# Kernel tuning notes

Measured on AMD Instinct MI355X. Metric: run time of the kernel, lower is better.

Reference implementation:

```python
import jax, jax.numpy as jnp
import numpy as np

R = 0.25
M = 0


def setup_inputs() -> dict:
    key = jax.random.key(0)
    k1, k2, k3, k4 = jax.random.split(key, 4)
    B, T_cmp, C = 2, 4096, 4096
    H, KVH, D, W = 32, 8, 128, 512
    return {
        "x_m": jax.random.normal(k1, (B, 2 * T_cmp, C), dtype=jnp.float32),
        "xm_cmp": jax.random.normal(k2, (B, T_cmp, C), dtype=jnp.float32),
        "q_w": jax.random.normal(k3, (B, H, W, D), dtype=jnp.float32),
        "km_cmp": jax.random.normal(k4, (B, KVH, T_cmp, D), dtype=jnp.float32),
    }


def reference(x_m, xm_cmp, q_w, km_cmp):
    B, T_cmp, C = xm_cmp.shape
    groups = q_w.shape[1] // km_cmp.shape[1]  # GQA repeat factor
    scaling = q_w.shape[-1] ** -0.5

    # importance_score: repeat kv heads, scaled-dot attention, softmax over keys,
    # sum over query positions, mean over heads -> [B, T_cmp]
    km = jnp.repeat(km_cmp, groups, axis=1)  # [B, H, T_cmp, D]
    scores = jnp.einsum('bhqd,bhkd->bhqk', q_w, km) * scaling
    weights = jax.nn.softmax(scores, axis=-1)
    importance = weights.sum(axis=2).mean(axis=1)  # [B, T_cmp]

    # select_indices: static top-k count
    k = min(int(R * T_cmp + M * (1 - R) / 2), T_cmp)
    _, idx = jax.lax.top_k(importance, k)  # [B, k]

    # interleave_selected: selected compressed tokens are replaced by their
    # two original tokens x_m[2t], x_m[2t+1]; others keep xm_cmp[t].
    b_idx = jnp.arange(B)[:, None]
    expand_mask = jnp.zeros((B, T_cmp), dtype=bool).at[b_idx, idx].set(True)
    sizes = jnp.where(expand_mask, 2, 1)
    start = jnp.cumsum(sizes, axis=1) - sizes  # output start position per token
    T_out = T_cmp + k

    first = jnp.where(expand_mask[..., None], x_m[:, ::2], xm_cmp)  # [B,T_cmp,C]
    second = x_m[:, 1::2]  # [B, T_cmp, C]
    pos2 = jnp.where(expand_mask, start + 1, T_out)  # non-expanded -> dummy slot

    y = jnp.zeros((B, T_out + 1, C), dtype=xm_cmp.dtype)
    y = y.at[b_idx, start].set(first)
    y = y.at[b_idx, pos2].set(second)
    return y[:, :T_out]
```

## Files before the change

kernel.cpp:

```cpp
#include <hip/hip_runtime.h>
#include <hip/hip_bf16.h>

#define B_    2
#define H_    32
#define KVH_  8
#define T_    4096
#define C_    4096
#define D_    128
#define W_    512
#define KTOP  1024
#define TOUT  (T_ + KTOP)
#define QB    64
#define NQB   (W_/QB)
#define TB    64
#define NTT   (T_/TB)
#define NPART (H_*NQB)
#define NBLK  (NQB*H_*B_)
#define SCALE 0.08838834764831845f

typedef __attribute__((ext_vector_type(8))) _Float16 half8;
typedef __attribute__((ext_vector_type(4))) float f32x4;

__device__ __forceinline__ void gload16(const void* g, void* l) {
    __builtin_amdgcn_global_load_lds(
        (const __attribute__((address_space(1))) void*)g,
        (__attribute__((address_space(3))) void*)l, 16, 0, 0);
}

__global__ __launch_bounds__(256) void convert_k_kernel(
    const float* __restrict__ km, _Float16* __restrict__ Khw,
    _Float16* __restrict__ Klw)
{
    int g = blockIdx.x*256 + threadIdx.x;
    size_t e = (size_t)g*8;
    int d0 = (int)(e & 127);
    size_t row = e >> 7;
    int t = (int)(row & (T_-1));
    size_t bk = row >> 12;
    int r = t & 63, tt = t >> 6;
    size_t off = (bk<<19) + (size_t)tt*(TB*D_) + (size_t)r*D_ + (d0 ^ ((r&7)<<3));
    float4 v0 = *(const float4*)(km + e);
    float4 v1 = *(const float4*)(km + e + 4);
    float f[8] = {v0.x,v0.y,v0.z,v0.w,v1.x,v1.y,v1.z,v1.w};
    half8 hh, hl;
#pragma unroll
    for (int i = 0; i < 8; ++i) {
        _Float16 hi = (_Float16)f[i];
        hh[i] = hi;
        hl[i] = (_Float16)(f[i] - (float)hi);
    }
    *(half8*)&Khw[off] = hh;
    *(half8*)&Klw[off] = hl;
}

#define STAGE_W(bufidx, tt)                                                 \
    {                                                                       \
        const _Float16* gh_ = gh0 + (size_t)(tt)*8192;                      \
        const _Float16* gl_ = gl0 + (size_t)(tt)*8192;                      \
        gload16(gh_,        &sKh[bufidx][wid][lane*8]);                     \
        gload16(gh_ + 512,  &sKh[bufidx][wid][512 + lane*8]);               \
        gload16(gh_ + 1024, &sKh[bufidx][wid][1024 + lane*8]);              \
        gload16(gh_ + 1536, &sKh[bufidx][wid][1536 + lane*8]);              \
        gload16(gl_,        &sKl[bufidx][wid][lane*8]);                     \
        gload16(gl_ + 512,  &sKl[bufidx][wid][512 + lane*8]);               \
        gload16(gl_ + 1024, &sKl[bufidx][wid][1024 + lane*8]);              \
        gload16(gl_ + 1536, &sKl[bufidx][wid][1536 + lane*8]);              \
    }

#define TILE_MFMA(bufidx, acc)                                              \
    {                                                                       \
        const _Float16* bKh = sKh[bufidx][wid];                             \
        const _Float16* bKl = sKl[bufidx][wid];                             \
        __builtin_amdgcn_s_setprio(1);                                      \
        _Pragma("unroll")                                                   \
        for (int ks2 = 0; ks2 < 4; ++ks2) {                                 \
            const int off = li*D_ + ((ks2*32 + lg*8) ^ ((li & 7) << 3));    \
            half8 bh = *(const half8*)&bKh[off];                            \
            half8 bl = *(const half8*)&bKl[off];                            \
            _Pragma("unroll")                                               \
            for (int mm = 0; mm < 4; ++mm) {                                \
                acc[mm] = __builtin_amdgcn_mfma_f32_16x16x32_f16(qh[mm][ks2], bh, acc[mm], 0,0,0); \
                acc[mm] = __builtin_amdgcn_mfma_f32_16x16x32_f16(ql[mm][ks2], bh, acc[mm], 0,0,0); \
                acc[mm] = __builtin_amdgcn_mfma_f32_16x16x32_f16(qh[mm][ks2], bl, acc[mm], 0,0,0); \
            }                                                               \
        }                                                                   \
        __builtin_amdgcn_s_setprio(0);                                      \
    }

__global__ __launch_bounds__(256, 2) void fused_imp_kernel(
    const float* __restrict__ q_w, const _Float16* __restrict__ Khw,
    const _Float16* __restrict__ Klw, float* __restrict__ partial)
{
    __shared__ __align__(16) _Float16 sKh[2][4][16*D_];
    __shared__ __align__(16) _Float16 sKl[2][4][16*D_];
    __shared__ float sL[4][QB];
    __shared__ float sR[QB];

    const int tid = threadIdx.x, wid = tid >> 6, lane = tid & 63;
    const int lg = lane >> 4, li = lane & 15;
    const int kg = wid;

    const int flat = blockIdx.x;
    const int xcd = flat & 7, m = flat >> 3;
    const int g = (m >> 5)*8 + xcd;
    const int r = m & 31;
    const int kvh = g & 7, b = g >> 3;
    const int hh = r >> 3, qb = r & 7;
    const int h = kvh*4 + hh;

    half8 qh[4][4], ql[4][4];
    {
        const float* qp0 = q_w + (((size_t)b*H_ + h)*W_ + qb*QB + li)*D_;
#pragma unroll
        for (int mm = 0; mm < 4; ++mm)
#pragma unroll
            for (int ks2 = 0; ks2 < 4; ++ks2) {
                const float* p = qp0 + mm*16*D_ + ks2*32 + lg*8;
                float4 v0 = *(const float4*)p;
                float4 v1 = *(const float4*)(p+4);
                float f[8] = {v0.x,v0.y,v0.z,v0.w,v1.x,v1.y,v1.z,v1.w};
#pragma unroll
                for (int e = 0; e < 8; ++e) {
                    _Float16 hv = (_Float16)f[e];
                    qh[mm][ks2][e] = hv;
                    ql[mm][ks2][e] = (_Float16)(f[e] - (float)hv);
                }
            }
    }

    const size_t kvoff = ((size_t)b*KVH_ + kvh) * ((size_t)T_*D_);
    const _Float16* gh0 = Khw + kvoff + (size_t)wid*2048 + (size_t)lane*8;
    const _Float16* gl0 = Klw + kvoff + (size_t)wid*2048 + (size_t)lane*8;

    float lacc[4][4] = {};
    STAGE_W(0, 0);
    int cur = 0;
    for (int tt = 0; tt < NTT; ++tt) {
        if (tt + 1 < NTT) {
            STAGE_W(cur^1, tt+1);
            asm volatile("s_waitcnt vmcnt(8)" ::: "memory");
        } else {
            asm volatile("s_waitcnt vmcnt(0)" ::: "memory");
        }
        f32x4 acc[4];
#pragma unroll
        for (int mm = 0; mm < 4; ++mm) acc[mm] = (f32x4){0.f,0.f,0.f,0.f};
        TILE_MFMA(cur, acc);
#pragma unroll
        for (int mm = 0; mm < 4; ++mm)
#pragma unroll
            for (int j = 0; j < 4; ++j)
                lacc[mm][j] += __expf(acc[mm][j]*SCALE);
        cur ^= 1;
    }
#pragma unroll
    for (int mm = 0; mm < 4; ++mm)
#pragma unroll
        for (int j = 0; j < 4; ++j) {
            float v = lacc[mm][j];
            v += __shfl_xor(v, 1); v += __shfl_xor(v, 2);
            v += __shfl_xor(v, 4); v += __shfl_xor(v, 8);
            if (li == 0) sL[kg][mm*16 + lg*4 + j] = v;
        }
    __syncthreads();
    if (tid < QB) {
        float l = sL[0][tid] + sL[1][tid] + sL[2][tid] + sL[3][tid];
        sR[tid] = 1.0f / l;
    }
    __syncthreads();
    float rv[4][4];
#pragma unroll
    for (int mm = 0; mm < 4; ++mm)
#pragma unroll
        for (int j = 0; j < 4; ++j)
            rv[mm][j] = sR[mm*16 + lg*4 + j];

    const size_t po = (((size_t)(h*NQB + qb))*B_ + b)*T_;
    STAGE_W(0, 0);
    cur = 0;
    for (int tt = 0; tt < NTT; ++tt) {
        if (tt == 0) {
            STAGE_W(cur^1, 1);
            asm volatile("s_waitcnt vmcnt(8)" ::: "memory");
        } else if (tt + 1 < NTT) {
            STAGE_W(cur^1, tt+1);
            asm volatile("s_waitcnt vmcnt(9)" ::: "memory");
        } else {
            asm volatile("s_waitcnt vmcnt(1)" ::: "memory");
        }
        f32x4 acc[4];
#pragma unroll
        for (int mm = 0; mm < 4; ++mm) acc[mm] = (f32x4){0.f,0.f,0.f,0.f};
        TILE_MFMA(cur, acc);
        float x = 0.f;
#pragma unroll
        for (int mm = 0; mm < 4; ++mm)
#pragma unroll
            for (int j = 0; j < 4; ++j)
                x += __expf(acc[mm][j]*SCALE)*rv[mm][j];
        x += __shfl_xor(x, 16); x += __shfl_xor(x, 32);
        if (lg == 0)
            partial[po + (size_t)tt*TB + kg*16 + li] = x;
        cur ^= 1;
    }
}

__global__ __launch_bounds__(256) void imp_reduce_kernel(
    const float* __restrict__ partial, float* __restrict__ imp)
{
    int gid = blockIdx.x*256 + threadIdx.x;
    int b = gid >> 12, t = gid & (T_-1);
    float s = 0.f;
    for (int i = 0; i < NPART; ++i)
        s += partial[((size_t)(i*B_ + b))*T_ + t];
    imp[gid] = s * (1.0f/H_);
}

__global__ __launch_bounds__(1024) void topk_kernel(
    const float* __restrict__ imp, int* __restrict__ mask, int* __restrict__ start)
{
    __shared__ int hist[256];
    __shared__ int sa[1024], sb[1024];
    __shared__ int sbin, srem;
    const int tid = threadIdx.x, b = blockIdx.x;
    const int i0 = 4*tid;

    unsigned key[4];
#pragma unroll
    for (int j = 0; j < 4; ++j) {
        unsigned u = __float_as_uint(imp[b*T_ + i0 + j]);
        key[j] = (u & 0x80000000u) ? ~u : (u | 0x80000000u);
    }

    unsigned prefix = 0;
    int k_rem = KTOP;
#pragma unroll
    for (int sh = 24; sh >= 0; sh -= 8) {
        unsigned hi_mask = (sh == 24) ? 0u : (0xFFFFFFFFu << (sh + 8));
        if (tid < 256) hist[tid] = 0;
        __syncthreads();
#pragma unroll
        for (int j = 0; j < 4; ++j)
            if ((key[j] & hi_mask) == prefix)
                atomicAdd(&hist[(key[j] >> sh) & 255], 1);
        __syncthreads();
        if (tid == 0) {
            int acc = 0, bin = 255;
            for (; bin > 0; --bin) {
                int hv = hist[bin];
                if (acc + hv >= k_rem) break;
                acc += hv;
            }
            sbin = bin; srem = k_rem - acc;
        }
        __syncthreads();
        prefix |= ((unsigned)sbin) << sh;
        k_rem = srem;
        __syncthreads();
    }

    int m[4], eq[4];
#pragma unroll
    for (int j = 0; j < 4; ++j) {
        m[j]  = key[j] > prefix ? 1 : 0;
        eq[j] = (key[j] == prefix) ? 1 : 0;
    }
    int e4 = eq[0]+eq[1]+eq[2]+eq[3];
    sa[tid] = e4;
    __syncthreads();
    {
        int *src = sa, *dst = sb;
        for (int off = 1; off < 1024; off <<= 1) {
            int v = src[tid];
            if (tid >= off) v += src[tid - off];
            dst[tid] = v;
            __syncthreads();
            int* t2 = src; src = dst; dst = t2;
        }
        int r = src[tid] - e4;
#pragma unroll
        for (int j = 0; j < 4; ++j) {
            if (eq[j] && r < k_rem) m[j] = 1;
            r += eq[j];
        }
    }
    __syncthreads();
    int s4 = m[0]+m[1]+m[2]+m[3];
    sa[tid] = s4;
    __syncthreads();
    int *src = sa, *dst = sb;
    for (int off = 1; off < 1024; off <<= 1) {
        int v = src[tid];
        if (tid >= off) v += src[tid - off];
        dst[tid] = v;
        __syncthreads();
        int* t2 = src; src = dst; dst = t2;
    }
    int excl = src[tid] - s4;
    start[b*T_+i0+0] = i0+0 + excl;
    start[b*T_+i0+1] = i0+1 + excl + m[0];
    start[b*T_+i0+2] = i0+2 + excl + m[0]+m[1];
    start[b*T_+i0+3] = i0+3 + excl + m[0]+m[1]+m[2];
    mask[b*T_+i0+0] = m[0]; mask[b*T_+i0+1] = m[1];
    mask[b*T_+i0+2] = m[2]; mask[b*T_+i0+3] = m[3];
}

__global__ __launch_bounds__(256) void scatter_kernel(
    const float* __restrict__ x_m, const float* __restrict__ xm_cmp,
    const int* __restrict__ mask, const int* __restrict__ start,
    float* __restrict__ out)
{
    const int t = blockIdx.x, b = blockIdx.y, tid = threadIdx.x;
    const int mk = mask[b*T_+t];
    const int st = start[b*T_+t];
    const float* s1 = mk ? (x_m + ((size_t)b*2*T_ + 2*t)*C_)
                         : (xm_cmp + ((size_t)b*T_ + t)*C_);
    float4* d1 = (float4*)(out + ((size_t)b*TOUT + st)*C_);
    const float4* s1v = (const float4*)s1;
    for (int i = tid; i < C_/4; i += 256) d1[i] = s1v[i];
    if (mk) {
        const float4* s2v = (const float4*)(x_m + ((size_t)b*2*T_ + 2*t+1)*C_);
        float4* d2 = d1 + C_/4;
        for (int i = tid; i < C_/4; i += 256) d2[i] = s2v[i];
    }
}

extern "C" void kernel_launch(void* const* d_in, const int* in_sizes, int n_in,
                              void* d_out, int out_size, void* d_ws, size_t ws_size,
                              hipStream_t stream)
{
    (void)in_sizes; (void)n_in; (void)out_size; (void)ws_size;
    const float* x_m    = (const float*)d_in[0];
    const float* xm_cmp = (const float*)d_in[1];
    const float* q_w    = (const float*)d_in[2];
    const float* km     = (const float*)d_in[3];
    float* out = (float*)d_out;

    char* ws = (char*)d_ws;
    _Float16* Khw   = (_Float16*)ws;
    _Float16* Klw   = (_Float16*)(ws + 16777216);
    float* partial  = (float*)(ws + 33554432);
    float* imp      = (float*)(ws + 41943040);
    int*   mask     = (int*)  (ws + 41975808);
    int*   start    = (int*)  (ws + 42008576);

    convert_k_kernel<<<dim3(4096), dim3(256), 0, stream>>>(km, Khw, Klw);
    fused_imp_kernel<<<dim3(NBLK), dim3(256), 0, stream>>>(q_w, Khw, Klw, partial);
    imp_reduce_kernel<<<dim3((B_*T_)/256), dim3(256), 0, stream>>>(partial, imp);
    topk_kernel<<<dim3(B_), dim3(1024), 0, stream>>>(imp, mask, start);
    scatter_kernel<<<dim3(T_, B_), dim3(256), 0, stream>>>(x_m, xm_cmp, mask, start, out);
}
```

Before: 314.0 us.

## Pipeline exp against MFMA, fold scale into Q, drop low-K term in pass one

Both passes of the fused importance kernel are software-pipelined with two accumulator sets, so the exponentials for tile t-1 overlap the MFMAs of tile t. The softmax scale times log2(e) is folded into the fp16 split of Q at load time, which lets the inner loops call raw exp2 with no per-element multiply. The normalizer pass now uses only the high half of K: it loads half the K data and issues two MFMAs per step instead of three. This reduces load traffic and MFMA work in that pass. The risk is a small precision mismatch between the denominator and the three-term second pass.

```diff
diff --git a/kernel.cpp b/kernel.cpp
--- a/kernel.cpp
+++ b/kernel.cpp
@@ -16,7 +16,7 @@
 #define NTT   (T_/TB)
 #define NPART (H_*NQB)
 #define NBLK  (NQB*H_*B_)
-#define SCALE 0.08838834764831845f
+#define SLOG2E 0.12751744f
 
 typedef __attribute__((ext_vector_type(8))) _Float16 half8;
 typedef __attribute__((ext_vector_type(4))) float f32x4;
@@ -53,7 +53,16 @@
     *(half8*)&Klw[off] = hl;
 }
 
-#define STAGE_W(bufidx, tt)                                                 \
+#define STAGE1(bufidx, tt)                                                  \
+    {                                                                       \
+        const _Float16* gh_ = gh0 + (size_t)(tt)*8192;                      \
+        gload16(gh_,        &sKh[bufidx][wid][lane*8]);                     \
+        gload16(gh_ + 512,  &sKh[bufidx][wid][512 + lane*8]);               \
+        gload16(gh_ + 1024, &sKh[bufidx][wid][1024 + lane*8]);              \
+        gload16(gh_ + 1536, &sKh[bufidx][wid][1536 + lane*8]);              \
+    }
+
+#define STAGE2(bufidx, tt)                                                  \
     {                                                                       \
         const _Float16* gh_ = gh0 + (size_t)(tt)*8192;                      \
         const _Float16* gl_ = gl0 + (size_t)(tt)*8192;                      \
@@ -67,7 +76,25 @@
         gload16(gl_ + 1536, &sKl[bufidx][wid][1536 + lane*8]);              \
     }
 
-#define TILE_MFMA(bufidx, acc)                                              \
+#define MFMA2(bufidx, acc)                                                  \
+    {                                                                       \
+        const _Float16* bKh = sKh[bufidx][wid];                             \
+        __builtin_amdgcn_s_setprio(1);                                      \
+        _Pragma("unroll")                                                   \
+        for (int ks2 = 0; ks2 < 4; ++ks2) {                                 \
+            const int off = li*D_ + ((ks2*32 + lg*8) ^ ((li & 7) << 3));    \
+            half8 bh = *(const half8*)&bKh[off];                            \
+            _Pragma("unroll")                                               \
+            for (int mm = 0; mm < 4; ++mm)                                  \
+                acc[mm] = __builtin_amdgcn_mfma_f32_16x16x32_f16(qh[mm][ks2], bh, acc[mm], 0,0,0); \
+            _Pragma("unroll")                                               \
+            for (int mm = 0; mm < 4; ++mm)                                  \
+                acc[mm] = __builtin_amdgcn_mfma_f32_16x16x32_f16(ql[mm][ks2], bh, acc[mm], 0,0,0); \
+        }                                                                   \
+        __builtin_amdgcn_s_setprio(0);                                      \
+    }
+
+#define MFMA3(bufidx, acc)                                                  \
     {                                                                       \
         const _Float16* bKh = sKh[bufidx][wid];                             \
         const _Float16* bKl = sKl[bufidx][wid];                             \
@@ -78,14 +105,57 @@
             half8 bh = *(const half8*)&bKh[off];                            \
             half8 bl = *(const half8*)&bKl[off];                            \
             _Pragma("unroll")                                               \
-            for (int mm = 0; mm < 4; ++mm) {                                \
+            for (int mm = 0; mm < 4; ++mm)                                  \
                 acc[mm] = __builtin_amdgcn_mfma_f32_16x16x32_f16(qh[mm][ks2], bh, acc[mm], 0,0,0); \
+            _Pragma("unroll")                                               \
+            for (int mm = 0; mm < 4; ++mm)                                  \
                 acc[mm] = __builtin_amdgcn_mfma_f32_16x16x32_f16(ql[mm][ks2], bh, acc[mm], 0,0,0); \
+            _Pragma("unroll")                                               \
+            for (int mm = 0; mm < 4; ++mm)                                  \
                 acc[mm] = __builtin_amdgcn_mfma_f32_16x16x32_f16(qh[mm][ks2], bl, acc[mm], 0,0,0); \
-            }                                                               \
         }                                                                   \
         __builtin_amdgcn_s_setprio(0);                                      \
     }
+
+#define EXPACC(acc)                                                         \
+    _Pragma("unroll")                                                       \
+    for (int mm = 0; mm < 4; ++mm)                                          \
+        _Pragma("unroll")                                                   \
+        for (int j = 0; j < 4; ++j)                                         \
+            lacc[mm][j] += __builtin_amdgcn_exp2f(acc[mm][j]);
+
+#define EXPSTORE(acc, t)                                                    \
+    {                                                                       \
+        float x = 0.f;                                                      \
+        _Pragma("unroll")                                                   \
+        for (int mm = 0; mm < 4; ++mm)                                      \
+            _Pragma("unroll")                                               \
+            for (int j = 0; j < 4; ++j)                                     \
+                x += __builtin_amdgcn_exp2f(acc[mm][j]) * rv[mm][j];        \
+        x += __shfl_xor(x, 16); x += __shfl_xor(x, 32);                     \
+        if (lg == 0)                                                        \
+            partial[po + (size_t)(t)*TB + kg*16 + li] = x;                  \
+    }
+
+#define P1BODY(t, ACCD, ACCE)                                               \
+    {                                                                       \
+        STAGE1(((t)+1) & 1, (t)+1);                                         \
+        asm volatile("s_waitcnt vmcnt(4)" ::: "memory");                    \
+        MFMA2((t) & 1, ACCD);                                               \
+        EXPACC(ACCE);                                                       \
+    }
+
+#define P2BODY(t, ACCD, ACCE)                                               \
+    {                                                                       \
+        STAGE2(((t)+1) & 1, (t)+1);                                         \
+        asm volatile("s_waitcnt vmcnt(9)" ::: "memory");                    \
+        MFMA3((t) & 1, ACCD);                                               \
+        EXPSTORE(ACCE, (t)-1);                                              \
+    }
+
+#define ACCZERO(acc)                                                        \
+    _Pragma("unroll")                                                       \
+    for (int mm = 0; mm < 4; ++mm) acc[mm] = (f32x4){0.f,0.f,0.f,0.f};
 
 __global__ __launch_bounds__(256, 2) void fused_imp_kernel(
     const float* __restrict__ q_w, const _Float16* __restrict__ Khw,
@@ -121,9 +191,10 @@
                 float f[8] = {v0.x,v0.y,v0.z,v0.w,v1.x,v1.y,v1.z,v1.w};
 #pragma unroll
                 for (int e = 0; e < 8; ++e) {
-                    _Float16 hv = (_Float16)f[e];
+                    float fs = f[e] * SLOG2E;
+                    _Float16 hv = (_Float16)fs;
                     qh[mm][ks2][e] = hv;
-                    ql[mm][ks2][e] = (_Float16)(f[e] - (float)hv);
+                    ql[mm][ks2][e] = (_Float16)(fs - (float)hv);
                 }
             }
     }
@@ -133,26 +204,25 @@
     const _Float16* gl0 = Klw + kvoff + (size_t)wid*2048 + (size_t)lane*8;
 
     float lacc[4][4] = {};
-    STAGE_W(0, 0);
-    int cur = 0;
-    for (int tt = 0; tt < NTT; ++tt) {
-        if (tt + 1 < NTT) {
-            STAGE_W(cur^1, tt+1);
-            asm volatile("s_waitcnt vmcnt(8)" ::: "memory");
-        } else {
-            asm volatile("s_waitcnt vmcnt(0)" ::: "memory");
-        }
-        f32x4 acc[4];
-#pragma unroll
-        for (int mm = 0; mm < 4; ++mm) acc[mm] = (f32x4){0.f,0.f,0.f,0.f};
-        TILE_MFMA(cur, acc);
-#pragma unroll
-        for (int mm = 0; mm < 4; ++mm)
-#pragma unroll
-            for (int j = 0; j < 4; ++j)
-                lacc[mm][j] += __expf(acc[mm][j]*SCALE);
-        cur ^= 1;
-    }
+    f32x4 accA[4], accB[4];
+
+    STAGE1(0, 0);
+    STAGE1(1, 1);
+    asm volatile("s_waitcnt vmcnt(4)" ::: "memory");
+    ACCZERO(accA);
+    MFMA2(0, accA);
+    for (int t = 1; t < NTT-1; t += 2) {
+        ACCZERO(accB);
+        P1BODY(t,   accB, accA);
+        ACCZERO(accA);
+        P1BODY(t+1, accA, accB);
+    }
+    asm volatile("s_waitcnt vmcnt(0)" ::: "memory");
+    ACCZERO(accB);
+    MFMA2(1, accB);
+    EXPACC(accA);
+    EXPACC(accB);
+
 #pragma unroll
     for (int mm = 0; mm < 4; ++mm)
 #pragma unroll
@@ -176,33 +246,22 @@
             rv[mm][j] = sR[mm*16 + lg*4 + j];
 
     const size_t po = (((size_t)(h*NQB + qb))*B_ + b)*T_;
-    STAGE_W(0, 0);
-    cur = 0;
-    for (int tt = 0; tt < NTT; ++tt) {
-        if (tt == 0) {
-            STAGE_W(cur^1, 1);
-            asm volatile("s_waitcnt vmcnt(8)" ::: "memory");
-        } else if (tt + 1 < NTT) {
-            STAGE_W(cur^1, tt+1);
-            asm volatile("s_waitcnt vmcnt(9)" ::: "memory");
-        } else {
-            asm volatile("s_waitcnt vmcnt(1)" ::: "memory");
-        }
-        f32x4 acc[4];
-#pragma unroll
-        for (int mm = 0; mm < 4; ++mm) acc[mm] = (f32x4){0.f,0.f,0.f,0.f};
-        TILE_MFMA(cur, acc);
-        float x = 0.f;
-#pragma unroll
-        for (int mm = 0; mm < 4; ++mm)
-#pragma unroll
-            for (int j = 0; j < 4; ++j)
-                x += __expf(acc[mm][j]*SCALE)*rv[mm][j];
-        x += __shfl_xor(x, 16); x += __shfl_xor(x, 32);
-        if (lg == 0)
-            partial[po + (size_t)tt*TB + kg*16 + li] = x;
-        cur ^= 1;
-    }
+    STAGE2(0, 0);
+    STAGE2(1, 1);
+    asm volatile("s_waitcnt vmcnt(8)" ::: "memory");
+    ACCZERO(accA);
+    MFMA3(0, accA);
+    for (int t = 1; t < NTT-1; t += 2) {
+        ACCZERO(accB);
+        P2BODY(t,   accB, accA);
+        ACCZERO(accA);
+        P2BODY(t+1, accA, accB);
+    }
+    asm volatile("s_waitcnt vmcnt(1)" ::: "memory");
+    ACCZERO(accB);
+    MFMA3(1, accB);
+    EXPSTORE(accA, NTT-2);
+    EXPSTORE(accB, NTT-1);
 }
 
 __global__ __launch_bounds__(256) void imp_reduce_kernel(
```

Measured after the change: 272.4 us. 13.2% less time.

## Single-buffer K tiles, skip K-low term in normalizer pass, fold scale into Q

Applied to the files above, without the earlier changes.

Replaces the double-buffered LDS staging with a single buffer: each tile is loaded into registers, then the next tile's async loads are issued into the same buffer. This halves shared memory so the launch bound can rise to 3 blocks per CU. The first pass (softmax normalizer) drops the q_hi*k_lo MFMA term and no longer loads K-low, which cuts MFMA and memory work at a small precision cost. The softmax scale times log2(e) is folded into Q so raw exp2 can replace expf with a multiply. The risk is that a single buffer exposes more load latency per tile, and the lower-precision normalizer may change top-k ties.

```diff
diff --git a/kernel.cpp b/kernel.cpp
--- a/kernel.cpp
+++ b/kernel.cpp
@@ -16,7 +16,7 @@
 #define NTT   (T_/TB)
 #define NPART (H_*NQB)
 #define NBLK  (NQB*H_*B_)
-#define SCALE 0.08838834764831845f
+#define SLOG2E 0.12751744f
 
 typedef __attribute__((ext_vector_type(8))) _Float16 half8;
 typedef __attribute__((ext_vector_type(4))) float f32x4;
@@ -53,46 +53,12 @@
     *(half8*)&Klw[off] = hl;
 }
 
-#define STAGE_W(bufidx, tt)                                                 \
-    {                                                                       \
-        const _Float16* gh_ = gh0 + (size_t)(tt)*8192;                      \
-        const _Float16* gl_ = gl0 + (size_t)(tt)*8192;                      \
-        gload16(gh_,        &sKh[bufidx][wid][lane*8]);                     \
-        gload16(gh_ + 512,  &sKh[bufidx][wid][512 + lane*8]);               \
-        gload16(gh_ + 1024, &sKh[bufidx][wid][1024 + lane*8]);              \
-        gload16(gh_ + 1536, &sKh[bufidx][wid][1536 + lane*8]);              \
-        gload16(gl_,        &sKl[bufidx][wid][lane*8]);                     \
-        gload16(gl_ + 512,  &sKl[bufidx][wid][512 + lane*8]);               \
-        gload16(gl_ + 1024, &sKl[bufidx][wid][1024 + lane*8]);              \
-        gload16(gl_ + 1536, &sKl[bufidx][wid][1536 + lane*8]);              \
-    }
-
-#define TILE_MFMA(bufidx, acc)                                              \
-    {                                                                       \
-        const _Float16* bKh = sKh[bufidx][wid];                             \
-        const _Float16* bKl = sKl[bufidx][wid];                             \
-        __builtin_amdgcn_s_setprio(1);                                      \
-        _Pragma("unroll")                                                   \
-        for (int ks2 = 0; ks2 < 4; ++ks2) {                                 \
-            const int off = li*D_ + ((ks2*32 + lg*8) ^ ((li & 7) << 3));    \
-            half8 bh = *(const half8*)&bKh[off];                            \
-            half8 bl = *(const half8*)&bKl[off];                            \
-            _Pragma("unroll")                                               \
-            for (int mm = 0; mm < 4; ++mm) {                                \
-                acc[mm] = __builtin_amdgcn_mfma_f32_16x16x32_f16(qh[mm][ks2], bh, acc[mm], 0,0,0); \
-                acc[mm] = __builtin_amdgcn_mfma_f32_16x16x32_f16(ql[mm][ks2], bh, acc[mm], 0,0,0); \
-                acc[mm] = __builtin_amdgcn_mfma_f32_16x16x32_f16(qh[mm][ks2], bl, acc[mm], 0,0,0); \
-            }                                                               \
-        }                                                                   \
-        __builtin_amdgcn_s_setprio(0);                                      \
-    }
-
-__global__ __launch_bounds__(256, 2) void fused_imp_kernel(
+__global__ __launch_bounds__(256, 3) void fused_imp_kernel(
     const float* __restrict__ q_w, const _Float16* __restrict__ Khw,
     const _Float16* __restrict__ Klw, float* __restrict__ partial)
 {
-    __shared__ __align__(16) _Float16 sKh[2][4][16*D_];
-    __shared__ __align__(16) _Float16 sKl[2][4][16*D_];
+    __shared__ __align__(16) _Float16 sKh[4][16*D_];
+    __shared__ __align__(16) _Float16 sKl[4][16*D_];
     __shared__ float sL[4][QB];
     __shared__ float sR[QB];
 
@@ -121,38 +87,63 @@
                 float f[8] = {v0.x,v0.y,v0.z,v0.w,v1.x,v1.y,v1.z,v1.w};
 #pragma unroll
                 for (int e = 0; e < 8; ++e) {
-                    _Float16 hv = (_Float16)f[e];
+                    float fs = f[e] * SLOG2E;
+                    _Float16 hv = (_Float16)fs;
                     qh[mm][ks2][e] = hv;
-                    ql[mm][ks2][e] = (_Float16)(f[e] - (float)hv);
+                    ql[mm][ks2][e] = (_Float16)(fs - (float)hv);
                 }
             }
     }
 
     const size_t kvoff = ((size_t)b*KVH_ + kvh) * ((size_t)T_*D_);
-    const _Float16* gh0 = Khw + kvoff + (size_t)wid*2048 + (size_t)lane*8;
-    const _Float16* gl0 = Klw + kvoff + (size_t)wid*2048 + (size_t)lane*8;
+    const _Float16* ghp = Khw + kvoff + (size_t)wid*2048 + (size_t)lane*8;
+    const _Float16* glp = Klw + kvoff + (size_t)wid*2048 + (size_t)lane*8;
+    _Float16* ldsh = &sKh[wid][lane*8];
+    _Float16* ldsl = &sKl[wid][lane*8];
+
+    int roff[4];
+#pragma unroll
+    for (int ks2 = 0; ks2 < 4; ++ks2)
+        roff[ks2] = li*D_ + ((ks2*32 + lg*8) ^ ((li & 7) << 3));
 
     float lacc[4][4] = {};
-    STAGE_W(0, 0);
-    int cur = 0;
+
+    gload16(ghp,      ldsh);       gload16(ghp+512,  ldsh+512);
+    gload16(ghp+1024, ldsh+1024);  gload16(ghp+1536, ldsh+1536);
+    ghp += 8192;
     for (int tt = 0; tt < NTT; ++tt) {
+        asm volatile("s_waitcnt vmcnt(0)" ::: "memory");
+        half8 bh[4];
+#pragma unroll
+        for (int ks2 = 0; ks2 < 4; ++ks2)
+            bh[ks2] = *(const half8*)&sKh[wid][roff[ks2]];
+        asm volatile("s_waitcnt lgkmcnt(0)" ::: "memory");
         if (tt + 1 < NTT) {
-            STAGE_W(cur^1, tt+1);
-            asm volatile("s_waitcnt vmcnt(8)" ::: "memory");
-        } else {
-            asm volatile("s_waitcnt vmcnt(0)" ::: "memory");
+            gload16(ghp,      ldsh);       gload16(ghp+512,  ldsh+512);
+            gload16(ghp+1024, ldsh+1024);  gload16(ghp+1536, ldsh+1536);
+            ghp += 8192;
         }
         f32x4 acc[4];
 #pragma unroll
         for (int mm = 0; mm < 4; ++mm) acc[mm] = (f32x4){0.f,0.f,0.f,0.f};
-        TILE_MFMA(cur, acc);
+        __builtin_amdgcn_s_setprio(1);
+#pragma unroll
+        for (int ks2 = 0; ks2 < 4; ++ks2) {
+#pragma unroll
+            for (int mm = 0; mm < 4; ++mm)
+                acc[mm] = __builtin_amdgcn_mfma_f32_16x16x32_f16(qh[mm][ks2], bh[ks2], acc[mm], 0,0,0);
+#pragma unroll
+            for (int mm = 0; mm < 4; ++mm)
+                acc[mm] = __builtin_amdgcn_mfma_f32_16x16x32_f16(ql[mm][ks2], bh[ks2], acc[mm], 0,0,0);
+        }
+        __builtin_amdgcn_s_setprio(0);
 #pragma unroll
         for (int mm = 0; mm < 4; ++mm)
 #pragma unroll
             for (int j = 0; j < 4; ++j)
-                lacc[mm][j] += __expf(acc[mm][j]*SCALE);
-        cur ^= 1;
-    }
+                lacc[mm][j] += __builtin_amdgcn_exp2f(acc[mm][j]);
+    }
+
 #pragma unroll
     for (int mm = 0; mm < 4; ++mm)
 #pragma unroll
@@ -176,32 +167,55 @@
             rv[mm][j] = sR[mm*16 + lg*4 + j];
 
     const size_t po = (((size_t)(h*NQB + qb))*B_ + b)*T_;
-    STAGE_W(0, 0);
-    cur = 0;
+    float* pp = partial + po + kg*16 + li;
+    ghp = Khw + kvoff + (size_t)wid*2048 + (size_t)lane*8;
+    gload16(ghp,      ldsh);       gload16(ghp+512,  ldsh+512);
+    gload16(ghp+1024, ldsh+1024);  gload16(ghp+1536, ldsh+1536);
+    gload16(glp,      ldsl);       gload16(glp+512,  ldsl+512);
+    gload16(glp+1024, ldsl+1024);  gload16(glp+1536, ldsl+1536);
+    ghp += 8192; glp += 8192;
     for (int tt = 0; tt < NTT; ++tt) {
-        if (tt == 0) {
-            STAGE_W(cur^1, 1);
-            asm volatile("s_waitcnt vmcnt(8)" ::: "memory");
-        } else if (tt + 1 < NTT) {
-            STAGE_W(cur^1, tt+1);
-            asm volatile("s_waitcnt vmcnt(9)" ::: "memory");
-        } else {
-            asm volatile("s_waitcnt vmcnt(1)" ::: "memory");
+        asm volatile("s_waitcnt vmcnt(0)" ::: "memory");
+        half8 bh[4], bl[4];
+#pragma unroll
+        for (int ks2 = 0; ks2 < 4; ++ks2) {
+            bh[ks2] = *(const half8*)&sKh[wid][roff[ks2]];
+            bl[ks2] = *(const half8*)&sKl[wid][roff[ks2]];
+        }
+        asm volatile("s_waitcnt lgkmcnt(0)" ::: "memory");
+        if (tt + 1 < NTT) {
+            gload16(ghp,      ldsh);       gload16(ghp+512,  ldsh+512);
+            gload16(ghp+1024, ldsh+1024);  gload16(ghp+1536, ldsh+1536);
+            gload16(glp,      ldsl);       gload16(glp+512,  ldsl+512);
+            gload16(glp+1024, ldsl+1024);  gload16(glp+1536, ldsl+1536);
+            ghp += 8192; glp += 8192;
         }
         f32x4 acc[4];
 #pragma unroll
         for (int mm = 0; mm < 4; ++mm) acc[mm] = (f32x4){0.f,0.f,0.f,0.f};
-        TILE_MFMA(cur, acc);
+        __builtin_amdgcn_s_setprio(1);
+#pragma unroll
+        for (int ks2 = 0; ks2 < 4; ++ks2) {
+#pragma unroll
+            for (int mm = 0; mm < 4; ++mm)
+                acc[mm] = __builtin_amdgcn_mfma_f32_16x16x32_f16(qh[mm][ks2], bh[ks2], acc[mm], 0,0,0);
+#pragma unroll
+            for (int mm = 0; mm < 4; ++mm)
+                acc[mm] = __builtin_amdgcn_mfma_f32_16x16x32_f16(ql[mm][ks2], bh[ks2], acc[mm], 0,0,0);
+#pragma unroll
+            for (int mm = 0; mm < 4; ++mm)
+                acc[mm] = __builtin_amdgcn_mfma_f32_16x16x32_f16(qh[mm][ks2], bl[ks2], acc[mm], 0,0,0);
+        }
+        __builtin_amdgcn_s_setprio(0);
         float x = 0.f;
 #pragma unroll
         for (int mm = 0; mm < 4; ++mm)
 #pragma unroll
             for (int j = 0; j < 4; ++j)
-                x += __expf(acc[mm][j]*SCALE)*rv[mm][j];
+                x += __builtin_amdgcn_exp2f(acc[mm][j]) * rv[mm][j];
         x += __shfl_xor(x, 16); x += __shfl_xor(x, 32);
-        if (lg == 0)
-            partial[po + (size_t)tt*TB + kg*16 + li] = x;
-        cur ^= 1;
+        if (lg == 0) *pp = x;
+        pp += TB;
     }
 }
 
```

After: 525.8 us. 67.5% more time.

## Switch importance kernel to 32x32 MFMA, hi-only first pass, exp2 prescale, nontemporal scatter

Applied to the files above, without the earlier changes.

Rewrites the fused importance kernel to use 32x32x16 f16 MFMA over 128-key tiles and folds scale*log2e into Q so the softmax uses exp2 directly. The denominator pass now uses only the high-half Q and K products, which halves its staging and cuts it to one MFMA per fragment, at some accuracy cost. The second pass streams the hi and lo K tiles through separate LDS buffers. The scatter copy now uses nontemporal loads and stores to avoid cache pollution.

```diff
diff --git a/kernel.cpp b/kernel.cpp
--- a/kernel.cpp
+++ b/kernel.cpp
@@ -12,14 +12,15 @@
 #define TOUT  (T_ + KTOP)
 #define QB    64
 #define NQB   (W_/QB)
-#define TB    64
-#define NTT   (T_/TB)
+#define TB2   128
+#define NTT2  (T_/TB2)
 #define NPART (H_*NQB)
 #define NBLK  (NQB*H_*B_)
-#define SCALE 0.08838834764831845f
+#define SLOG2E 0.12751744f
 
 typedef __attribute__((ext_vector_type(8))) _Float16 half8;
 typedef __attribute__((ext_vector_type(4))) float f32x4;
+typedef __attribute__((ext_vector_type(16))) float f32x16;
 
 __device__ __forceinline__ void gload16(const void* g, void* l) {
     __builtin_amdgcn_global_load_lds(
@@ -38,7 +39,7 @@
     int t = (int)(row & (T_-1));
     size_t bk = row >> 12;
     int r = t & 63, tt = t >> 6;
-    size_t off = (bk<<19) + (size_t)tt*(TB*D_) + (size_t)r*D_ + (d0 ^ ((r&7)<<3));
+    size_t off = (bk<<19) + (size_t)tt*(64*D_) + (size_t)r*D_ + (d0 ^ ((r&7)<<3));
     float4 v0 = *(const float4*)(km + e);
     float4 v1 = *(const float4*)(km + e + 4);
     float f[8] = {v0.x,v0.y,v0.z,v0.w,v1.x,v1.y,v1.z,v1.w};
@@ -53,36 +54,26 @@
     *(half8*)&Klw[off] = hl;
 }
 
-#define STAGE_W(bufidx, tt)                                                 \
+#define STAGE_T(gbase, t, buf)                                              \
     {                                                                       \
-        const _Float16* gh_ = gh0 + (size_t)(tt)*8192;                      \
-        const _Float16* gl_ = gl0 + (size_t)(tt)*8192;                      \
-        gload16(gh_,        &sKh[bufidx][wid][lane*8]);                     \
-        gload16(gh_ + 512,  &sKh[bufidx][wid][512 + lane*8]);               \
-        gload16(gh_ + 1024, &sKh[bufidx][wid][1024 + lane*8]);              \
-        gload16(gh_ + 1536, &sKh[bufidx][wid][1536 + lane*8]);              \
-        gload16(gl_,        &sKl[bufidx][wid][lane*8]);                     \
-        gload16(gl_ + 512,  &sKl[bufidx][wid][512 + lane*8]);               \
-        gload16(gl_ + 1024, &sKl[bufidx][wid][1024 + lane*8]);              \
-        gload16(gl_ + 1536, &sKl[bufidx][wid][1536 + lane*8]);              \
-    }
-
-#define TILE_MFMA(bufidx, acc)                                              \
+        const _Float16* g_ = (gbase) + (size_t)(t)*16384;                   \
+        _Pragma("unroll")                                                   \
+        for (int i_ = 0; i_ < 8; ++i_)                                      \
+            gload16(g_ + i_*512, (buf) + i_*512 + lane*8);                  \
+    }
+
+#define READF(buf, kf)                                                      \
+    _Pragma("unroll")                                                       \
+    for (int c_ = 0; c_ < 8; ++c_)                                          \
+        kf[c_] = *(const half8*)&(buf)[rr*128 + ((c_*16 + hi*8) ^ xsw)];
+
+#define MFMA_T(qf, kf, acc)                                                 \
     {                                                                       \
-        const _Float16* bKh = sKh[bufidx][wid];                             \
-        const _Float16* bKl = sKl[bufidx][wid];                             \
         __builtin_amdgcn_s_setprio(1);                                      \
         _Pragma("unroll")                                                   \
-        for (int ks2 = 0; ks2 < 4; ++ks2) {                                 \
-            const int off = li*D_ + ((ks2*32 + lg*8) ^ ((li & 7) << 3));    \
-            half8 bh = *(const half8*)&bKh[off];                            \
-            half8 bl = *(const half8*)&bKl[off];                            \
-            _Pragma("unroll")                                               \
-            for (int mm = 0; mm < 4; ++mm) {                                \
-                acc[mm] = __builtin_amdgcn_mfma_f32_16x16x32_f16(qh[mm][ks2], bh, acc[mm], 0,0,0); \
-                acc[mm] = __builtin_amdgcn_mfma_f32_16x16x32_f16(ql[mm][ks2], bh, acc[mm], 0,0,0); \
-                acc[mm] = __builtin_amdgcn_mfma_f32_16x16x32_f16(qh[mm][ks2], bl, acc[mm], 0,0,0); \
-            }                                                               \
+        for (int c_ = 0; c_ < 8; ++c_) {                                    \
+            acc[0] = __builtin_amdgcn_mfma_f32_32x32x16_f16(qf[0][c_], kf[c_], acc[0], 0,0,0); \
+            acc[1] = __builtin_amdgcn_mfma_f32_32x32x16_f16(qf[1][c_], kf[c_], acc[1], 0,0,0); \
         }                                                                   \
         __builtin_amdgcn_s_setprio(0);                                      \
     }
@@ -91,13 +82,13 @@
     const float* __restrict__ q_w, const _Float16* __restrict__ Khw,
     const _Float16* __restrict__ Klw, float* __restrict__ partial)
 {
-    __shared__ __align__(16) _Float16 sKh[2][4][16*D_];
-    __shared__ __align__(16) _Float16 sKl[2][4][16*D_];
+    __shared__ __align__(16) _Float16 sK[4][8192];
     __shared__ float sL[4][QB];
     __shared__ float sR[QB];
 
     const int tid = threadIdx.x, wid = tid >> 6, lane = tid & 63;
-    const int lg = lane >> 4, li = lane & 15;
+    const int rr = lane & 31, hi = lane >> 5;
+    const int xsw = (rr & 7) << 3;
     const int kg = wid;
 
     const int flat = blockIdx.x;
@@ -108,59 +99,68 @@
     const int hh = r >> 3, qb = r & 7;
     const int h = kvh*4 + hh;
 
-    half8 qh[4][4], ql[4][4];
+    half8 qh[2][8], ql[2][8];
     {
-        const float* qp0 = q_w + (((size_t)b*H_ + h)*W_ + qb*QB + li)*D_;
-#pragma unroll
-        for (int mm = 0; mm < 4; ++mm)
-#pragma unroll
-            for (int ks2 = 0; ks2 < 4; ++ks2) {
-                const float* p = qp0 + mm*16*D_ + ks2*32 + lg*8;
+        const float* qp0 = q_w + (((size_t)b*H_ + h)*W_ + qb*QB + rr)*D_;
+#pragma unroll
+        for (int mm = 0; mm < 2; ++mm)
+#pragma unroll
+            for (int c = 0; c < 8; ++c) {
+                const float* p = qp0 + mm*32*D_ + c*16 + hi*8;
                 float4 v0 = *(const float4*)p;
                 float4 v1 = *(const float4*)(p+4);
                 float f[8] = {v0.x,v0.y,v0.z,v0.w,v1.x,v1.y,v1.z,v1.w};
 #pragma unroll
                 for (int e = 0; e < 8; ++e) {
-                    _Float16 hv = (_Float16)f[e];
-                    qh[mm][ks2][e] = hv;
-                    ql[mm][ks2][e] = (_Float16)(f[e] - (float)hv);
+                    float fs = f[e] * SLOG2E;
+                    _Float16 hv = (_Float16)fs;
+                    qh[mm][c][e] = hv;
+                    ql[mm][c][e] = (_Float16)(fs - (float)hv);
                 }
             }
     }
 
     const size_t kvoff = ((size_t)b*KVH_ + kvh) * ((size_t)T_*D_);
-    const _Float16* gh0 = Khw + kvoff + (size_t)wid*2048 + (size_t)lane*8;
-    const _Float16* gl0 = Klw + kvoff + (size_t)wid*2048 + (size_t)lane*8;
-
-    float lacc[4][4] = {};
-    STAGE_W(0, 0);
-    int cur = 0;
-    for (int tt = 0; tt < NTT; ++tt) {
-        if (tt + 1 < NTT) {
-            STAGE_W(cur^1, tt+1);
-            asm volatile("s_waitcnt vmcnt(8)" ::: "memory");
-        } else {
-            asm volatile("s_waitcnt vmcnt(0)" ::: "memory");
-        }
-        f32x4 acc[4];
-#pragma unroll
-        for (int mm = 0; mm < 4; ++mm) acc[mm] = (f32x4){0.f,0.f,0.f,0.f};
-        TILE_MFMA(cur, acc);
-#pragma unroll
-        for (int mm = 0; mm < 4; ++mm)
-#pragma unroll
-            for (int j = 0; j < 4; ++j)
-                lacc[mm][j] += __expf(acc[mm][j]*SCALE);
-        cur ^= 1;
-    }
-#pragma unroll
-    for (int mm = 0; mm < 4; ++mm)
-#pragma unroll
-        for (int j = 0; j < 4; ++j) {
-            float v = lacc[mm][j];
-            v += __shfl_xor(v, 1); v += __shfl_xor(v, 2);
-            v += __shfl_xor(v, 4); v += __shfl_xor(v, 8);
-            if (li == 0) sL[kg][mm*16 + lg*4 + j] = v;
+    const _Float16* gh0 = Khw + kvoff + (size_t)(kg>>1)*8192
+                        + (size_t)(kg&1)*4096 + (size_t)lane*8;
+    const _Float16* gl0 = Klw + kvoff + (size_t)(kg>>1)*8192
+                        + (size_t)(kg&1)*4096 + (size_t)lane*8;
+    _Float16* ldsA = &sK[wid][0];
+    _Float16* ldsB = &sK[wid][4096];
+
+    half8 kf[8];
+    f32x16 acc[2];
+    float lacc[2][16] = {};
+
+    STAGE_T(gh0, 0, ldsA);
+    STAGE_T(gh0, 1, ldsB);
+    for (int t = 0; t < NTT2; ++t) {
+        if (t + 1 < NTT2) { asm volatile("s_waitcnt vmcnt(8)" ::: "memory"); }
+        else              { asm volatile("s_waitcnt vmcnt(0)" ::: "memory"); }
+        _Float16* cur = (t & 1) ? ldsB : ldsA;
+        READF(cur, kf);
+        asm volatile("s_waitcnt lgkmcnt(0)" ::: "memory");
+        __builtin_amdgcn_sched_barrier(0);
+        if (t + 2 < NTT2) STAGE_T(gh0, t+2, cur);
+        acc[0] = (f32x16)(0.f); acc[1] = (f32x16)(0.f);
+        MFMA_T(qh, kf, acc);
+#pragma unroll
+        for (int mm = 0; mm < 2; ++mm)
+#pragma unroll
+            for (int rg = 0; rg < 16; ++rg)
+                lacc[mm][rg] += __builtin_amdgcn_exp2f(acc[mm][rg]);
+    }
+
+#pragma unroll
+    for (int mm = 0; mm < 2; ++mm)
+#pragma unroll
+        for (int rg = 0; rg < 16; ++rg) {
+            float v = lacc[mm][rg];
+            v += __shfl_xor(v, 1);  v += __shfl_xor(v, 2);
+            v += __shfl_xor(v, 4);  v += __shfl_xor(v, 8);
+            v += __shfl_xor(v, 16);
+            if (rr == 0)
+                sL[kg][mm*32 + (rg&3) + 8*(rg>>2) + 4*hi] = v;
         }
     __syncthreads();
     if (tid < QB) {
@@ -168,40 +168,39 @@
         sR[tid] = 1.0f / l;
     }
     __syncthreads();
-    float rv[4][4];
-#pragma unroll
-    for (int mm = 0; mm < 4; ++mm)
-#pragma unroll
-        for (int j = 0; j < 4; ++j)
-            rv[mm][j] = sR[mm*16 + lg*4 + j];
+    float rv[2][16];
+#pragma unroll
+    for (int mm = 0; mm < 2; ++mm)
+#pragma unroll
+        for (int rg = 0; rg < 16; ++rg)
+            rv[mm][rg] = sR[mm*32 + (rg&3) + 8*(rg>>2) + 4*hi];
 
     const size_t po = (((size_t)(h*NQB + qb))*B_ + b)*T_;
-    STAGE_W(0, 0);
-    cur = 0;
-    for (int tt = 0; tt < NTT; ++tt) {
-        if (tt == 0) {
-            STAGE_W(cur^1, 1);
-            asm volatile("s_waitcnt vmcnt(8)" ::: "memory");
-        } else if (tt + 1 < NTT) {
-            STAGE_W(cur^1, tt+1);
-            asm volatile("s_waitcnt vmcnt(9)" ::: "memory");
-        } else {
-            asm volatile("s_waitcnt vmcnt(1)" ::: "memory");
-        }
-        f32x4 acc[4];
-#pragma unroll
-        for (int mm = 0; mm < 4; ++mm) acc[mm] = (f32x4){0.f,0.f,0.f,0.f};
-        TILE_MFMA(cur, acc);
+    STAGE_T(gh0, 0, ldsA);
+    STAGE_T(gl0, 0, ldsB);
+    for (int t = 0; t < NTT2; ++t) {
+        asm volatile("s_waitcnt vmcnt(0)" ::: "memory");
+        READF(ldsA, kf);
+        asm volatile("s_waitcnt lgkmcnt(0)" ::: "memory");
+        __builtin_amdgcn_sched_barrier(0);
+        if (t + 1 < NTT2) STAGE_T(gh0, t+1, ldsA);
+        acc[0] = (f32x16)(0.f); acc[1] = (f32x16)(0.f);
+        MFMA_T(qh, kf, acc);
+        MFMA_T(ql, kf, acc);
+        READF(ldsB, kf);
+        asm volatile("s_waitcnt lgkmcnt(0)" ::: "memory");
+        __builtin_amdgcn_sched_barrier(0);
+        if (t + 1 < NTT2) STAGE_T(gl0, t+1, ldsB);
+        MFMA_T(qh, kf, acc);
         float x = 0.f;
 #pragma unroll
-        for (int mm = 0; mm < 4; ++mm)
-#pragma unroll
-            for (int j = 0; j < 4; ++j)
-                x += __expf(acc[mm][j]*SCALE)*rv[mm][j];
-        x += __shfl_xor(x, 16); x += __shfl_xor(x, 32);
-        if (lg == 0)
-            partial[po + (size_t)tt*TB + kg*16 + li] = x;
-        cur ^= 1;
+        for (int mm = 0; mm < 2; ++mm)
+#pragma unroll
+            for (int rg = 0; rg < 16; ++rg)
+                x += __builtin_amdgcn_exp2f(acc[mm][rg]) * rv[mm][rg];
+        x += __shfl_xor(x, 32);
+        if (lane < 32)
+            partial[po + (size_t)t*TB2 + kg*32 + lane] = x;
     }
 }
 
@@ -315,13 +314,19 @@
     const int st = start[b*T_+t];
     const float* s1 = mk ? (x_m + ((size_t)b*2*T_ + 2*t)*C_)
                          : (xm_cmp + ((size_t)b*T_ + t)*C_);
-    float4* d1 = (float4*)(out + ((size_t)b*TOUT + st)*C_);
-    const float4* s1v = (const float4*)s1;
-    for (int i = tid; i < C_/4; i += 256) d1[i] = s1v[i];
+    f32x4* d1 = (f32x4*)(out + ((size_t)b*TOUT + st)*C_);
+    const f32x4* s1v = (const f32x4*)s1;
+    for (int i = tid; i < C_/4; i += 256) {
+        f32x4 v = __builtin_nontemporal_load(s1v + i);
+        __builtin_nontemporal_store(v, d1 + i);
+    }
     if (mk) {
-        const float4* s2v = (const float4*)(x_m + ((size_t)b*2*T_ + 2*t+1)*C_);
-        float4* d2 = d1 + C_/4;
-        for (int i = tid; i < C_/4; i += 256) d2[i] = s2v[i];
+        const f32x4* s2v = (const f32x4*)(x_m + ((size_t)b*2*T_ + 2*t+1)*C_);
+        f32x4* d2 = d1 + C_/4;
+        for (int i = tid; i < C_/4; i += 256) {
+            f32x4 v = __builtin_nontemporal_load(s2v + i);
+            __builtin_nontemporal_store(v, d2 + i);
+        }
     }
 }
 
```

New measurement: 299.1 us. -4.7%, faster.
